# Performance work log

Hardware: AMD Instinct MI355X
Metric: run time of the kernel (lower is better)

Reference implementation:

```python
import jax, jax.numpy as jnp
import numpy as np

B, T, S, H = 4, 2048, 2048, 1024


def setup_inputs() -> dict:
    key = jax.random.key(0)
    k1, k2, k3, k4, k5, k6 = jax.random.split(key, 6)
    scale_w = 1.0 / np.sqrt(H)  # roughly nn.Linear init scale
    return {
        "tar": jax.random.normal(k1, (B, T, H), jnp.float32),
        "src": jax.random.normal(k2, (B, S, H), jnp.float32),
        "ori_src": jax.random.normal(k3, (B, S, H), jnp.float32),
        "Wq": jax.random.normal(k4, (H, H), jnp.float32) * scale_w,
        "Wk": jax.random.normal(k5, (H, H), jnp.float32) * scale_w,
        "Wv": jax.random.normal(k6, (H, H), jnp.float32) * scale_w,
    }


def reference(tar, src, ori_src, Wq, Wk, Wv):
    # nn.Linear(bias=False): y = x @ W.T
    q = src @ Wq.T        # (B, S, H)
    k = tar @ Wk.T        # (B, T, H)
    v = ori_src @ Wv.T    # (B, S, H)
    scaling = jnp.asarray(H ** 0.5, q.dtype)
    # scores[b,t,s] = q[b,s] . k[b,t] / sqrt(H); torch softmax was over dim=-2 (the S axis)
    scores = jnp.einsum('bsh,bth->bts', q, k) / scaling  # (B, T, S)
    attn = jax.nn.softmax(scores, axis=-1)               # softmax over src positions s
    context = jnp.einsum('bts,bsh->bth', attn, v)        # (B, T, H)
    return context, attn
```

## Files before the change

### kernel.cpp

```cpp
#include <hip/hip_runtime.h>

#define BB 4
#define TT 2048
#define SS 2048
#define HH 1024

typedef unsigned short u16;
typedef __attribute__((ext_vector_type(4))) unsigned short u16x4;
typedef __attribute__((ext_vector_type(8))) short bf16x8;
typedef __attribute__((ext_vector_type(4))) float f32x4;

#define TILE_U16 (128 * 32)

__device__ __forceinline__ u16 f2bf(float f) {
    union { float f; unsigned u; } a; a.f = f;
    unsigned r = a.u + 0x7fffu + ((a.u >> 16) & 1u);
    return (u16)(r >> 16);
}
__device__ __forceinline__ float bf2f(u16 h) {
    union { unsigned u; float f; } a; a.u = ((unsigned)h) << 16;
    return a.f;
}


__device__ __forceinline__ void stage_bf16(const u16* gbase, int ld, int row0, int k0,
                                           u16* lds, int tid) {
#pragma unroll
    for (int c = 0; c < 2; ++c) {
        int g = c * 256 + tid;
        int row = g >> 2, col = g & 3;
        const u16* gp = gbase + (size_t)(row0 + row) * ld + k0 + col * 8;
        u16* lp = lds + (size_t)(c * 256 + (tid & ~63)) * 8;
        __builtin_amdgcn_global_load_lds((__attribute__((address_space(1))) const void*)gp,
                                         (__attribute__((address_space(3))) void*)lp,
                                         16, 0, 0);
    }
}

__device__ __forceinline__ void stage_f32(const float* gbase, int ld, int row0, int k0,
                                          u16* lds, int tid) {
#pragma unroll
    for (int c = 0; c < 4; ++c) {
        int f = c * 256 + tid;
        int row = f >> 3, c4 = f & 7;
        const float4 v = *(const float4*)(gbase + (size_t)(row0 + row) * ld + k0 + c4 * 4);
        u16x4 o;
        o.x = f2bf(v.x); o.y = f2bf(v.y); o.z = f2bf(v.z); o.w = f2bf(v.w);
        *(u16x4*)(lds + row * 32 + c4 * 4) = o;
    }
}

__device__ __forceinline__ void mfma_step(const u16* As, const u16* Bs,
                                          f32x4 acc[4][4], int tid) {
    int lane = tid & 63, quad = lane >> 4, l16 = lane & 15;
    int wm = (tid >> 6) & 1, wn = tid >> 7;
    const u16* Ab = As + (wm * 64 + l16) * 32 + quad * 8;
    const u16* Bb = Bs + (wn * 64 + l16) * 32 + quad * 8;
    bf16x8 af[4], bfr[4];
#pragma unroll
    for (int i = 0; i < 4; ++i) af[i] = *(const bf16x8*)(Ab + i * 512);
#pragma unroll
    for (int j = 0; j < 4; ++j) bfr[j] = *(const bf16x8*)(Bb + j * 512);
#pragma unroll
    for (int i = 0; i < 4; ++i)
#pragma unroll
        for (int j = 0; j < 4; ++j)
            acc[i][j] = __builtin_amdgcn_mfma_f32_16x16x32_bf16(af[i], bfr[j], acc[i][j], 0, 0, 0);
}

__device__ __forceinline__ void zero_acc(f32x4 acc[4][4]) {
#pragma unroll
    for (int i = 0; i < 4; ++i)
#pragma unroll
        for (int j = 0; j < 4; ++j)
            acc[i][j] = (f32x4){0.f, 0.f, 0.f, 0.f};
}

__device__ __forceinline__ void gemm_loop_bf16(const u16* A, int lda, int bm,
                                               const u16* B, int ldb, int bn,
                                               int K, u16* As, u16* Bs,
                                               f32x4 acc[4][4], int tid) {
    stage_bf16(A, lda, bm, 0, As, tid);
    stage_bf16(B, ldb, bn, 0, Bs, tid);
    const int kiters = K / 32;
    for (int kit = 0; kit < kiters; ++kit) {
        const int cur = (kit & 1) * TILE_U16, nxt = TILE_U16 - cur;
        __syncthreads();
        if (kit + 1 < kiters) {
            stage_bf16(A, lda, bm, (kit + 1) * 32, As + nxt, tid);
            stage_bf16(B, ldb, bn, (kit + 1) * 32, Bs + nxt, tid);
        }
        mfma_step(As + cur, Bs + cur, acc, tid);
    }
}

__device__ __forceinline__ void gemm_loop_f32a(const float* A, int lda, int bm,
                                               const u16* B, int ldb, int bn,
                                               int K, u16* As, u16* Bs,
                                               f32x4 acc[4][4], int tid) {
    stage_f32(A, lda, bm, 0, As, tid);
    stage_bf16(B, ldb, bn, 0, Bs, tid);
    const int kiters = K / 32;
    for (int kit = 0; kit < kiters; ++kit) {
        const int cur = (kit & 1) * TILE_U16, nxt = TILE_U16 - cur;
        __syncthreads();
        if (kit + 1 < kiters) {
            stage_f32(A, lda, bm, (kit + 1) * 32, As + nxt, tid);
            stage_bf16(B, ldb, bn, (kit + 1) * 32, Bs + nxt, tid);
        }
        mfma_step(As + cur, Bs + cur, acc, tid);
    }
}


__global__ __launch_bounds__(256) void cvt3_kernel(const float* __restrict__ p0,
                                                   const float* __restrict__ p1,
                                                   const float* __restrict__ p2,
                                                   u16* __restrict__ o0,
                                                   u16* __restrict__ o1,
                                                   u16* __restrict__ o2) {
    const int z = blockIdx.y;
    const float* in = (z == 0) ? p0 : (z == 1) ? p1 : p2;
    u16* out = (z == 0) ? o0 : (z == 1) ? o1 : o2;
    int i = (blockIdx.x * 256 + threadIdx.x) * 4;
    float4 v = *(const float4*)(in + i);
    u16x4 o;
    o.x = f2bf(v.x); o.y = f2bf(v.y); o.z = f2bf(v.z); o.w = f2bf(v.w);
    *(u16x4*)(out + i) = o;
}

__global__ __launch_bounds__(256) void cvt_kernel(const float* __restrict__ in,
                                                  u16* __restrict__ out) {
    int i = (blockIdx.x * 256 + threadIdx.x) * 4;
    float4 v = *(const float4*)(in + i);
    u16x4 o;
    o.x = f2bf(v.x); o.y = f2bf(v.y); o.z = f2bf(v.z); o.w = f2bf(v.w);
    *(u16x4*)(out + i) = o;
}

__global__ __launch_bounds__(256) void zero_kernel(float* __restrict__ p) {
    int i = (blockIdx.x * 256 + threadIdx.x) * 4;
    *(float4*)(p + i) = (float4){0.f, 0.f, 0.f, 0.f};
}


__device__ __forceinline__ void stage_half(const u16* g, int ld, u16* lds, int tid) {
#pragma unroll
    for (int c = 0; c < 2; ++c) {
        int gr = c * 512 + tid;
        int r = gr >> 3, k8 = gr & 7;
        const u16* gp = g + (size_t)r * ld + ((k8 ^ (r & 7)) << 3);
        u16* lp = lds + (size_t)(c * 512 + (tid & ~63)) * 8;
        __builtin_amdgcn_global_load_lds((__attribute__((address_space(1))) const void*)gp,
                                         (__attribute__((address_space(3))) void*)lp,
                                         16, 0, 0);
    }
}

#define G_RD_A(dst, Abp, qm)                                                  \
    _Pragma("unroll") for (int i = 0; i < 4; ++i) {                           \
        const u16* _p = (Abp) + ((qm) * 64 + i * 16 + l16) * 64;              \
        dst[i][0] = *(const bf16x8*)(_p + co0);                               \
        dst[i][1] = *(const bf16x8*)(_p + co1);                               \
    }

#define G_RD_B(dst, Bbp, qn)                                                  \
    _Pragma("unroll") for (int j = 0; j < J2; ++j) {                          \
        const u16* _p = (Bbp) + (rB0 + (qn) * J2 * 16 + j * 16 + l16) * 64;   \
        dst[j][0] = *(const bf16x8*)(_p + co0);                               \
        dst[j][1] = *(const bf16x8*)(_p + co1);                               \
    }

#define G_MM(af, bf, qm, qn)                                                  \
    __builtin_amdgcn_s_setprio(1);                                            \
    _Pragma("unroll") for (int i = 0; i < 4; ++i)                             \
        _Pragma("unroll") for (int j = 0; j < J2; ++j) {                      \
            acc[(qm) * 4 + i][(qn) * J2 + j] =                                \
                __builtin_amdgcn_mfma_f32_16x16x32_bf16(                      \
                    af[i][0], bf[j][0], acc[(qm) * 4 + i][(qn) * J2 + j], 0, 0, 0); \
            acc[(qm) * 4 + i][(qn) * J2 + j] =                                \
                __builtin_amdgcn_mfma_f32_16x16x32_bf16(                      \
                    af[i][1], bf[j][1], acc[(qm) * 4 + i][(qn) * J2 + j], 0, 0, 0); \
        }                                                                     \
    __builtin_amdgcn_s_setprio(0);

template <int BN>
__device__ __forceinline__ void g256_loop(const u16* __restrict__ A, int lda,
                                          const u16* __restrict__ B, int ldb, int K,
                                          u16* sm, f32x4 (&acc)[8][BN / 64], int tid) {
    constexpr int J2 = BN / 128;
    constexpr int ATILE = 16384;
    constexpr int BTILE = BN * 64;
    u16* As = sm;
    u16* Bs = sm + 2 * ATILE;
    const int lane = tid & 63, wid = tid >> 6;
    const int wm = wid >> 2, wn = wid & 3;
    const int l16 = lane & 15, quad = lane >> 4;
    const int co0 = (quad ^ (l16 & 7)) * 8;
    const int co1 = ((4 | quad) ^ (l16 & 7)) * 8;
    const int rB0 = (BN == 256) ? (wn & 1) * 64 : wn * 32;
    const int NT = K >> 6;

#pragma unroll
    for (int i = 0; i < 8; ++i)
#pragma unroll
        for (int j = 0; j < BN / 64; ++j) acc[i][j] = (f32x4){0.f, 0.f, 0.f, 0.f};

    stage_half(A, lda, As, tid);
    stage_half(A + (size_t)128 * lda, lda, As + 8192, tid);
    stage_half(B, ldb, Bs, tid);
    if (BN == 256) stage_half(B + (size_t)128 * ldb, ldb, Bs + 8192, tid);
    stage_half(A + 64, lda, As + ATILE, tid);
    stage_half(A + (size_t)128 * lda + 64, lda, As + ATILE + 8192, tid);
    asm volatile("s_waitcnt vmcnt(4)" ::: "memory");
    __builtin_amdgcn_s_barrier();
    __builtin_amdgcn_sched_barrier(0);

    const u16* Aw = As + wm * 8192;
    const u16* Bw = Bs + ((BN == 256) ? (wn >> 1) * 8192 : 0);

    bf16x8 a0[4][2], a1[4][2], b0[J2][2], b1[J2][2];
    {
        const u16* Ab = Aw;
        const u16* Bb = Bw;
        G_RD_A(a0, Ab, 0)
        G_RD_B(b0, Bb, 0)
    }

    for (int t = 0; t < NT; ++t) {
        const u16* Ab = Aw + (t & 1) * ATILE;
        const u16* Bb = Bw + (t & 1) * BTILE;
        const int nx = (t + 1) & 1;
        G_RD_A(a1, Ab, 1)
        if (t + 1 < NT) stage_half(B + (size_t)(t + 1) * 64, ldb, Bs + nx * BTILE, tid);
        __builtin_amdgcn_sched_barrier(0);
        G_MM(a0, b0, 0, 0)
        G_RD_B(b1, Bb, 1)
        if (BN == 256 && t + 1 < NT)
            stage_half(B + (size_t)128 * ldb + (size_t)(t + 1) * 64, ldb,
                       Bs + nx * BTILE + 8192, tid);
        __builtin_amdgcn_sched_barrier(0);
        G_MM(a1, b0, 1, 0)
        asm volatile("s_waitcnt lgkmcnt(0)" ::: "memory");
        __builtin_amdgcn_sched_barrier(0);
        __builtin_amdgcn_s_barrier();
        if (t + 2 < NT) {
            stage_half(A + (size_t)(t + 2) * 64, lda, As + (t & 1) * ATILE, tid);
            stage_half(A + (size_t)128 * lda + (size_t)(t + 2) * 64, lda,
                       As + (t & 1) * ATILE + 8192, tid);
        }
        __builtin_amdgcn_sched_barrier(0);
        G_MM(a0, b1, 0, 1)
        if (t + 2 < NT) asm volatile("s_waitcnt vmcnt(4)" ::: "memory");
        else            asm volatile("s_waitcnt vmcnt(0)" ::: "memory");
        __builtin_amdgcn_s_barrier();
        __builtin_amdgcn_sched_barrier(0);
        if (t + 1 < NT) {
            const u16* An = Aw + nx * ATILE;
            const u16* Bn = Bw + nx * BTILE;
            G_RD_A(a0, An, 0)
            G_RD_B(b0, Bn, 0)
        }
        __builtin_amdgcn_sched_barrier(0);
        G_MM(a1, b1, 1, 1)
    }
}

__global__ __launch_bounds__(512, 2) void proj256_kernel(
        const u16* __restrict__ A0, const u16* __restrict__ A1, const u16* __restrict__ A2,
        const u16* __restrict__ W0, const u16* __restrict__ W1, const u16* __restrict__ W2,
        u16* __restrict__ qb, u16* __restrict__ kb, u16* __restrict__ vT) {
    __shared__ u16 sm[2 * 16384 + 2 * 128 * 64];
    const int bid = blockIdx.x;
    const int wg = (bid & 7) * 96 + (bid >> 3);
    const int z = wg >> 8, rr = wg & 255;
    const int by = rr >> 3, bx = rr & 7;
    const u16* A = ((z == 0) ? A0 : (z == 1) ? A1 : A2) + (size_t)(by * 256) * HH;
    const u16* W = ((z == 0) ? W0 : (z == 1) ? W1 : W2) + (size_t)(bx * 128) * HH;
    const int tid = threadIdx.x;
    f32x4 acc[8][2];
    g256_loop<128>(A, HH, W, HH, HH, sm, acc, tid);

    const int lane = tid & 63, quad = lane >> 4, l16 = lane & 15, wid = tid >> 6;
    const int wm = wid >> 2, wn = wid & 3;
    const int m0 = by * 256 + wm * 128, n0 = bx * 128 + wn * 32;
    if (z < 2) {
        u16* C = z ? kb : qb;
#pragma unroll
        for (int i = 0; i < 8; ++i)
#pragma unroll
            for (int j = 0; j < 2; ++j) {
                const int m = m0 + i * 16 + quad * 4;
                const int n = n0 + j * 16 + l16;
#pragma unroll
                for (int r = 0; r < 4; ++r)
                    C[(size_t)(m + r) * HH + n] = f2bf(acc[i][j][r]);
            }
    } else {
#pragma unroll
        for (int i = 0; i < 8; ++i)
#pragma unroll
            for (int j = 0; j < 2; ++j) {
                const int m = m0 + i * 16 + quad * 4;
                const int n = n0 + j * 16 + l16;
                u16x4 o;
                o.x = f2bf(acc[i][j][0]); o.y = f2bf(acc[i][j][1]);
                o.z = f2bf(acc[i][j][2]); o.w = f2bf(acc[i][j][3]);
                *(u16x4*)(vT + (size_t)n * (BB * SS) + m) = o;
            }
    }
}

__global__ __launch_bounds__(512, 2) void scores256_kernel(
        const u16* __restrict__ qb, const u16* __restrict__ kb,
        u16* __restrict__ eb, float* __restrict__ rowsum) {
    __shared__ u16 sm[2 * 16384 + 2 * 256 * 64];
    const int bid = blockIdx.x;
    const int wg = (bid & 7) * 32 + (bid >> 3);
    const int b = wg >> 6, by = (wg >> 3) & 7, bx = wg & 7;
    const u16* A = kb + (size_t)b * TT * HH + (size_t)(by * 256) * HH;
    const u16* Q = qb + (size_t)b * SS * HH + (size_t)(bx * 256) * HH;
    const int tid = threadIdx.x;
    f32x4 acc[8][4];
    g256_loop<256>(A, HH, Q, HH, HH, sm, acc, tid);

    const int lane = tid & 63, quad = lane >> 4, l16 = lane & 15, wid = tid >> 6;
    const int wm = wid >> 2, wn = wid & 3;
    const int m0 = by * 256 + wm * 128, n0 = bx * 256 + wn * 64;
#pragma unroll
    for (int i = 0; i < 8; ++i)
#pragma unroll
        for (int j = 0; j < 4; ++j)
#pragma unroll
            for (int r = 0; r < 4; ++r)
                acc[i][j][r] = __expf(acc[i][j][r] * 0.03125f);
    u16* E = eb + (size_t)b * TT * SS;
#pragma unroll
    for (int i = 0; i < 8; ++i)
#pragma unroll
        for (int j = 0; j < 4; ++j) {
            const int m = m0 + i * 16 + quad * 4;
            const int n = n0 + j * 16 + l16;
#pragma unroll
            for (int r = 0; r < 4; ++r)
                E[(size_t)(m + r) * SS + n] = f2bf(acc[i][j][r]);
        }
    const size_t Rb = (size_t)b * TT + m0 + quad * 4;
#pragma unroll
    for (int i = 0; i < 8; ++i)
#pragma unroll
        for (int r = 0; r < 4; ++r) {
            float s = acc[i][0][r] + acc[i][1][r] + acc[i][2][r] + acc[i][3][r];
            s += __shfl_xor(s, 1, 64);
            s += __shfl_xor(s, 2, 64);
            s += __shfl_xor(s, 4, 64);
            s += __shfl_xor(s, 8, 64);
            if (l16 == 0) atomicAdd(&rowsum[Rb + i * 16 + r], s);
        }
}

__global__ __launch_bounds__(512, 2) void ctx256_kernel(
        const u16* __restrict__ eb, const u16* __restrict__ vT,
        const float* __restrict__ rowsum, float* __restrict__ out) {
    __shared__ u16 sm[2 * 16384 + 2 * 128 * 64];
    const int bid = blockIdx.x;
    const int wg = (bid & 7) * 32 + (bid >> 3);
    const int b = wg >> 6, by = (wg >> 3) & 7, bx = wg & 7;
    const u16* A = eb + (size_t)b * TT * SS + (size_t)(by * 256) * SS;
    const u16* V = vT + (size_t)b * SS + (size_t)(bx * 128) * (size_t)(BB * SS);
    const int tid = threadIdx.x;
    f32x4 acc[8][2];
    g256_loop<128>(A, SS, V, BB * SS, SS, sm, acc, tid);

    const int lane = tid & 63, quad = lane >> 4, l16 = lane & 15, wid = tid >> 6;
    const int wm = wid >> 2, wn = wid & 3;
    const int m0 = by * 256 + wm * 128, n0 = bx * 128 + wn * 32;
    float* C = out + (size_t)b * TT * HH;
    const float* RS = rowsum + (size_t)b * TT;
#pragma unroll
    for (int i = 0; i < 8; ++i)
#pragma unroll
        for (int r = 0; r < 4; ++r) {
            const int m = m0 + i * 16 + quad * 4 + r;
            const float scl = 1.0f / RS[m];
#pragma unroll
            for (int j = 0; j < 2; ++j)
                C[(size_t)m * HH + n0 + j * 16 + l16] = acc[i][j][r] * scl;
        }
}


template <int AF32, int NZ>
__global__ __launch_bounds__(256, 4) void proj_kernel(const float* __restrict__ F0,
                                                      const float* __restrict__ F1,
                                                      const float* __restrict__ F2,
                                                      const u16* __restrict__ A0,
                                                      const u16* __restrict__ A1,
                                                      const u16* __restrict__ A2,
                                                      const u16* __restrict__ W0,
                                                      const u16* __restrict__ W1,
                                                      const u16* __restrict__ W2,
                                                      u16* __restrict__ qb,
                                                      u16* __restrict__ kb,
                                                      u16* __restrict__ vT,
                                                      int zbase) {
    __shared__ u16 As[2 * TILE_U16];
    __shared__ u16 Bs[2 * TILE_U16];
    const int bid = blockIdx.x;
    const int xcd = bid & 7, slot = bid >> 3;
    const int bx = slot & 7;
    const int grp = xcd * (NZ * 8) + (slot >> 3);
    const int z = zbase + (NZ == 3 ? (grp >> 6) : 0);
    const int by = grp & 63;

    const float* AF = (z == 0) ? F0 : (z == 1) ? F1 : F2;
    const u16* AB = (z == 0) ? A0 : (z == 1) ? A1 : A2;
    const u16* W = (z == 0) ? W0 : (z == 1) ? W1 : W2;
    const int bm = by * 128, bn = bx * 128;
    const int tid = threadIdx.x;

    f32x4 acc[4][4];
    zero_acc(acc);
    if (AF32) gemm_loop_f32a(AF, HH, bm, W, HH, bn, HH, As, Bs, acc, tid);
    else      gemm_loop_bf16(AB, HH, bm, W, HH, bn, HH, As, Bs, acc, tid);

    const int lane = tid & 63, quad = lane >> 4, l16 = lane & 15;
    const int wm = (tid >> 6) & 1, wn = tid >> 7;
    const int m0 = bm + wm * 64, n0 = bn + wn * 64;
    if (z < 2) {
        u16* C = (z == 0) ? qb : kb;
#pragma unroll
        for (int i = 0; i < 4; ++i)
#pragma unroll
            for (int j = 0; j < 4; ++j) {
                int m = m0 + i * 16 + quad * 4;
                int n = n0 + j * 16 + l16;
#pragma unroll
                for (int r = 0; r < 4; ++r)
                    C[(size_t)(m + r) * HH + n] = f2bf(acc[i][j][r]);
            }
    } else {
#pragma unroll
        for (int i = 0; i < 4; ++i)
#pragma unroll
            for (int j = 0; j < 4; ++j) {
                int m = m0 + i * 16 + quad * 4;
                int n = n0 + j * 16 + l16;
                u16x4 o;
                o.x = f2bf(acc[i][j][0]); o.y = f2bf(acc[i][j][1]);
                o.z = f2bf(acc[i][j][2]); o.w = f2bf(acc[i][j][3]);
                *(u16x4*)(vT + (size_t)n * (BB * SS) + m) = o;
            }
    }
}

template <int FUSE>
__global__ __launch_bounds__(256, 4) void scores_kernel(const u16* __restrict__ qb,
                                                        const u16* __restrict__ kb,
                                                        float* __restrict__ attn,
                                                        u16* __restrict__ eb,
                                                        float* __restrict__ rowsum) {
    __shared__ u16 As[2 * TILE_U16];
    __shared__ u16 Bs[2 * TILE_U16];
    const int bid = blockIdx.x;
    const int xcd = bid & 7, slot = bid >> 3;
    const int bx = slot & 15;
    const int grp = xcd * 8 + (slot >> 4);
    const int b = grp >> 4, by = grp & 15;

    const u16* A = kb + (size_t)b * TT * HH;
    const u16* Bq = qb + (size_t)b * SS * HH;
    const int bm = by * 128, bn = bx * 128;
    const int tid = threadIdx.x;

    f32x4 acc[4][4];
    zero_acc(acc);
    gemm_loop_bf16(A, HH, bm, Bq, HH, bn, HH, As, Bs, acc, tid);

    const int lane = tid & 63, quad = lane >> 4, l16 = lane & 15;
    const int wm = (tid >> 6) & 1, wn = tid >> 7;
    const int m0 = bm + wm * 64, n0 = bn + wn * 64;

    if (FUSE) {
#pragma unroll
        for (int i = 0; i < 4; ++i)
#pragma unroll
            for (int j = 0; j < 4; ++j)
#pragma unroll
                for (int r = 0; r < 4; ++r)
                    acc[i][j][r] = __expf(acc[i][j][r] * 0.03125f);
        u16* E = eb + (size_t)b * TT * SS;
#pragma unroll
        for (int i = 0; i < 4; ++i)
#pragma unroll
            for (int j = 0; j < 4; ++j) {
                int m = m0 + i * 16 + quad * 4;
                int n = n0 + j * 16 + l16;
#pragma unroll
                for (int r = 0; r < 4; ++r)
                    E[(size_t)(m + r) * SS + n] = f2bf(acc[i][j][r]);
            }
        const size_t Rb = (size_t)b * TT + m0 + quad * 4;
#pragma unroll
        for (int i = 0; i < 4; ++i)
#pragma unroll
            for (int r = 0; r < 4; ++r) {
                float s = acc[i][0][r] + acc[i][1][r] + acc[i][2][r] + acc[i][3][r];
                s += __shfl_xor(s, 1, 64);
                s += __shfl_xor(s, 2, 64);
                s += __shfl_xor(s, 4, 64);
                s += __shfl_xor(s, 8, 64);
                if (l16 == 0) atomicAdd(&rowsum[Rb + i * 16 + r], s);
            }
    } else {
        float* C = attn + (size_t)b * TT * SS;
#pragma unroll
        for (int i = 0; i < 4; ++i)
#pragma unroll
            for (int j = 0; j < 4; ++j) {
                int m = m0 + i * 16 + quad * 4;
                int n = n0 + j * 16 + l16;
#pragma unroll
                for (int r = 0; r < 4; ++r)
                    C[(size_t)(m + r) * SS + n] = acc[i][j][r] * 0.03125f;
            }
    }
}

__global__ __launch_bounds__(256) void norm_kernel(const u16* __restrict__ eb,
                                                   const float* __restrict__ rowsum,
                                                   float* __restrict__ attn) {
    const size_t row = blockIdx.x;
    const float inv = 1.0f / rowsum[row];
    const u16* p = eb + row * SS;
    float* o = attn + row * SS;
    const int tid = threadIdx.x;
#pragma unroll
    for (int c = 0; c < 2; ++c) {
        u16x4 v = *(const u16x4*)(p + c * 1024 + tid * 4);
        float4 f;
        f.x = bf2f(v.x) * inv; f.y = bf2f(v.y) * inv;
        f.z = bf2f(v.z) * inv; f.w = bf2f(v.w) * inv;
        *(float4*)(o + c * 1024 + tid * 4) = f;
    }
}

__global__ __launch_bounds__(256) void softmax_kernel(float* __restrict__ attn,
                                                      u16* __restrict__ attn_bf) {
    const size_t row = blockIdx.x;
    float* p = attn + row * SS;
    const int tid = threadIdx.x;
    float4 a = *(float4*)(p + tid * 4);
    float4 b = *(float4*)(p + 1024 + tid * 4);

    float m = fmaxf(fmaxf(fmaxf(a.x, a.y), fmaxf(a.z, a.w)),
                    fmaxf(fmaxf(b.x, b.y), fmaxf(b.z, b.w)));
#pragma unroll
    for (int off = 32; off > 0; off >>= 1) m = fmaxf(m, __shfl_xor(m, off, 64));
    __shared__ float rmax[4], rsum[4];
    if ((tid & 63) == 0) rmax[tid >> 6] = m;
    __syncthreads();
    m = fmaxf(fmaxf(rmax[0], rmax[1]), fmaxf(rmax[2], rmax[3]));

    a.x = __expf(a.x - m); a.y = __expf(a.y - m);
    a.z = __expf(a.z - m); a.w = __expf(a.w - m);
    b.x = __expf(b.x - m); b.y = __expf(b.y - m);
    b.z = __expf(b.z - m); b.w = __expf(b.w - m);
    float s = a.x + a.y + a.z + a.w + b.x + b.y + b.z + b.w;
#pragma unroll
    for (int off = 32; off > 0; off >>= 1) s += __shfl_xor(s, off, 64);
    if ((tid & 63) == 0) rsum[tid >> 6] = s;
    __syncthreads();
    s = rsum[0] + rsum[1] + rsum[2] + rsum[3];
    float inv = 1.0f / s;

    a.x *= inv; a.y *= inv; a.z *= inv; a.w *= inv;
    b.x *= inv; b.y *= inv; b.z *= inv; b.w *= inv;
    *(float4*)(p + tid * 4) = a;
    *(float4*)(p + 1024 + tid * 4) = b;

    if (attn_bf) {
        u16* pb = attn_bf + row * SS;
        u16x4 oa, ob;
        oa.x = f2bf(a.x); oa.y = f2bf(a.y); oa.z = f2bf(a.z); oa.w = f2bf(a.w);
        ob.x = f2bf(b.x); ob.y = f2bf(b.y); ob.z = f2bf(b.z); ob.w = f2bf(b.w);
        *(u16x4*)(pb + tid * 4) = oa;
        *(u16x4*)(pb + 1024 + tid * 4) = ob;
    }
}

template <int AF32, int SCALE>
__global__ __launch_bounds__(256, 4) void ctx_kernel(const float* __restrict__ attnF,
                                                     const u16* __restrict__ attnB,
                                                     const u16* __restrict__ vT,
                                                     const float* __restrict__ rowsum,
                                                     float* __restrict__ out) {
    __shared__ u16 As[2 * TILE_U16];
    __shared__ u16 Bs[2 * TILE_U16];
    const int bid = blockIdx.x;
    const int xcd = bid & 7, slot = bid >> 3;
    const int bx = slot & 7;
    const int grp = xcd * 8 + (slot >> 3);
    const int b = grp >> 4, by = grp & 15;

    const float* AF = attnF + (size_t)b * TT * SS;
    const u16* AB = attnB + (size_t)b * TT * SS;
    const u16* Bv = vT + (size_t)b * SS;
    float* C = out + (size_t)b * TT * HH;
    const int bm = by * 128, bn = bx * 128;
    const int tid = threadIdx.x;

    f32x4 acc[4][4];
    zero_acc(acc);
    if (AF32) gemm_loop_f32a(AF, SS, bm, Bv, BB * SS, bn, SS, As, Bs, acc, tid);
    else      gemm_loop_bf16(AB, SS, bm, Bv, BB * SS, bn, SS, As, Bs, acc, tid);

    const int lane = tid & 63, quad = lane >> 4, l16 = lane & 15;
    const int wm = (tid >> 6) & 1, wn = tid >> 7;
    const int m0 = bm + wm * 64, n0 = bn + wn * 64;
#pragma unroll
    for (int i = 0; i < 4; ++i)
#pragma unroll
        for (int r = 0; r < 4; ++r) {
            int m = m0 + i * 16 + quad * 4 + r;
            float scl = 1.0f;
            if (SCALE) scl = 1.0f / rowsum[(size_t)b * TT + m];
#pragma unroll
            for (int j = 0; j < 4; ++j) {
                int n = n0 + j * 16 + l16;
                C[(size_t)m * HH + n] = acc[i][j][r] * scl;
            }
        }
}

extern "C" void kernel_launch(void* const* d_in, const int* in_sizes, int n_in,
                              void* d_out, int out_size, void* d_ws, size_t ws_size,
                              hipStream_t stream) {
    const float* tar = (const float*)d_in[0];
    const float* src = (const float*)d_in[1];
    const float* ori = (const float*)d_in[2];
    const float* Wq  = (const float*)d_in[3];
    const float* Wk  = (const float*)d_in[4];
    const float* Wv  = (const float*)d_in[5];

    float* ctx_out  = (float*)d_out;
    float* attn_out = ctx_out + (size_t)BB * TT * HH;

    const size_t M1 = 1024 * 1024;
    u16* ws  = (u16*)d_ws;
    u16* qb  = ws;
    u16* kb  = ws + 8 * M1;
    u16* vT  = ws + 16 * M1;
    u16* wqb = ws + 24 * M1;
    u16* wkb = ws + 25 * M1;
    u16* wvb = ws + 26 * M1;
    u16* inb = ws + 27 * M1;
    u16* eb = inb;
    float* rowsum = (float*)wqb;
    u16* attn_bf = qb;

    const size_t need_fused = (27 + 24) * M1 * 2;
    const size_t need_split = (27 + 8) * M1 * 2;
    const int mode = (ws_size >= need_fused) ? 0 : (ws_size >= need_split) ? 1 : 2;

    cvt3_kernel<<<dim3(1024, 3), 256, 0, stream>>>(Wq, Wk, Wv, wqb, wkb, wvb);

    if (mode == 0) {
        u16* srcb = inb;
        u16* tarb = inb + 8 * M1;
        u16* orib = inb + 16 * M1;
        cvt3_kernel<<<dim3(8192, 3), 256, 0, stream>>>(src, tar, ori, srcb, tarb, orib);
        proj256_kernel<<<768, 512, 0, stream>>>(srcb, tarb, orib, wqb, wkb, wvb, qb, kb, vT);
        zero_kernel<<<8, 256, 0, stream>>>(rowsum);
        scores256_kernel<<<256, 512, 0, stream>>>(qb, kb, eb, rowsum);
        norm_kernel<<<BB * TT, 256, 0, stream>>>(eb, rowsum, attn_out);
        ctx256_kernel<<<256, 512, 0, stream>>>(eb, vT, rowsum, ctx_out);
    } else if (mode == 1) {
        const float* fin[3] = {src, tar, ori};
        for (int z = 0; z < 3; ++z) {
            cvt_kernel<<<8192, 256, 0, stream>>>(fin[z], inb);
            proj_kernel<0, 1><<<512, 256, 0, stream>>>(
                nullptr, nullptr, nullptr, inb, inb, inb, wqb, wkb, wvb, qb, kb, vT, z);
        }
        scores_kernel<0><<<1024, 256, 0, stream>>>(qb, kb, attn_out, nullptr, nullptr);
        softmax_kernel<<<BB * TT, 256, 0, stream>>>(attn_out, attn_bf);
        ctx_kernel<0, 0><<<512, 256, 0, stream>>>(nullptr, attn_bf, vT, nullptr, ctx_out);
    } else {
        proj_kernel<1, 3><<<1536, 256, 0, stream>>>(
            src, tar, ori, nullptr, nullptr, nullptr, wqb, wkb, wvb, qb, kb, vT, 0);
        scores_kernel<0><<<1024, 256, 0, stream>>>(qb, kb, attn_out, nullptr, nullptr);
        softmax_kernel<<<BB * TT, 256, 0, stream>>>(attn_out, nullptr);
        ctx_kernel<1, 0><<<512, 256, 0, stream>>>(attn_out, nullptr, vT, nullptr, ctx_out);
    }
}
```

Before: 345.1 us.

## Restructure GEMM main loop schedule and use 256x256 tiles in projection

Rewrites the shared GEMM inner loop so each MFMA quadrant is preceded by a barrier-plus-lgkmcnt wait, with LDS fragment reads and global staging interleaved differently across the four sub-steps and no cross-iteration register prefetch. Separately, the projection kernel switches from 256x128 to 256x256 tiles, halving the grid to 384 blocks and doubling the LDS footprint and accumulators. The goal is better MFMA/LDS overlap and more data reuse in the projection. The cost is more barriers per iteration, more registers per thread, and lower block count and occupancy, since the loop change also affects the scores and context kernels that share it.

```diff
diff --git a/kernel.cpp b/kernel.cpp
--- a/kernel.cpp
+++ b/kernel.cpp
@@ -183,6 +183,12 @@
                     af[i][1], bf[j][1], acc[(qm) * 4 + i][(qn) * J2 + j], 0, 0, 0); \
         }                                                                     \
     __builtin_amdgcn_s_setprio(0);
+
+#define G_SYNC_PRE_MM()                                                       \
+    __builtin_amdgcn_sched_barrier(0);                                        \
+    __builtin_amdgcn_s_barrier();                                             \
+    asm volatile("s_waitcnt lgkmcnt(0)" ::: "memory");                        \
+    __builtin_amdgcn_sched_barrier(0);
 
 template <int BN>
 __device__ __forceinline__ void g256_loop(const u16* __restrict__ A, int lda,
@@ -216,53 +222,44 @@
     __builtin_amdgcn_s_barrier();
     __builtin_amdgcn_sched_barrier(0);
 
-    const u16* Aw = As + wm * 8192;
-    const u16* Bw = Bs + ((BN == 256) ? (wn >> 1) * 8192 : 0);
+    const u16* AwBase = As + wm * 8192;
+    const u16* BwBase = Bs + ((BN == 256) ? (wn >> 1) * 8192 : 0);
 
     bf16x8 a0[4][2], a1[4][2], b0[J2][2], b1[J2][2];
-    {
-        const u16* Ab = Aw;
-        const u16* Bb = Bw;
+
+    for (int t = 0; t < NT; ++t) {
+        const u16* Ab = AwBase + (t & 1) * ATILE;
+        const u16* Bb = BwBase + (t & 1) * BTILE;
+        const int curA = (t & 1) * ATILE;
+        const int nxB = ((t + 1) & 1) * BTILE;
         G_RD_A(a0, Ab, 0)
         G_RD_B(b0, Bb, 0)
-    }
-
-    for (int t = 0; t < NT; ++t) {
-        const u16* Ab = Aw + (t & 1) * ATILE;
-        const u16* Bb = Bw + (t & 1) * BTILE;
-        const int nx = (t + 1) & 1;
+        if (t + 1 < NT) stage_half(B + (size_t)(t + 1) * 64, ldb, Bs + nxB, tid);
+        G_SYNC_PRE_MM()
+        G_MM(a0, b0, 0, 0)
+        __builtin_amdgcn_s_barrier();
         G_RD_A(a1, Ab, 1)
-        if (t + 1 < NT) stage_half(B + (size_t)(t + 1) * 64, ldb, Bs + nx * BTILE, tid);
-        __builtin_amdgcn_sched_barrier(0);
-        G_MM(a0, b0, 0, 0)
-        G_RD_B(b1, Bb, 1)
         if (BN == 256 && t + 1 < NT)
             stage_half(B + (size_t)128 * ldb + (size_t)(t + 1) * 64, ldb,
-                       Bs + nx * BTILE + 8192, tid);
-        __builtin_amdgcn_sched_barrier(0);
+                       Bs + nxB + 8192, tid);
+        G_SYNC_PRE_MM()
         G_MM(a1, b0, 1, 0)
-        asm volatile("s_waitcnt lgkmcnt(0)" ::: "memory");
-        __builtin_amdgcn_sched_barrier(0);
         __builtin_amdgcn_s_barrier();
-        if (t + 2 < NT) {
-            stage_half(A + (size_t)(t + 2) * 64, lda, As + (t & 1) * ATILE, tid);
+        G_RD_B(b1, Bb, 1)
+        if (t + 2 < NT)
+            stage_half(A + (size_t)(t + 2) * 64, lda, As + curA, tid);
+        G_SYNC_PRE_MM()
+        G_MM(a1, b1, 1, 1)
+        __builtin_amdgcn_s_barrier();
+        if (t + 2 < NT)
             stage_half(A + (size_t)128 * lda + (size_t)(t + 2) * 64, lda,
-                       As + (t & 1) * ATILE + 8192, tid);
-        }
+                       As + curA + 8192, tid);
         __builtin_amdgcn_sched_barrier(0);
         G_MM(a0, b1, 0, 1)
-        if (t + 2 < NT) asm volatile("s_waitcnt vmcnt(4)" ::: "memory");
-        else            asm volatile("s_waitcnt vmcnt(0)" ::: "memory");
+        if (t + 2 < NT)      asm volatile("s_waitcnt vmcnt(4)" ::: "memory");
+        else if (t + 1 < NT) asm volatile("s_waitcnt vmcnt(0)" ::: "memory");
         __builtin_amdgcn_s_barrier();
         __builtin_amdgcn_sched_barrier(0);
-        if (t + 1 < NT) {
-            const u16* An = Aw + nx * ATILE;
-            const u16* Bn = Bw + nx * BTILE;
-            G_RD_A(a0, An, 0)
-            G_RD_B(b0, Bn, 0)
-        }
-        __builtin_amdgcn_sched_barrier(0);
-        G_MM(a1, b1, 1, 1)
     }
 }
 
@@ -270,26 +267,26 @@
         const u16* __restrict__ A0, const u16* __restrict__ A1, const u16* __restrict__ A2,
         const u16* __restrict__ W0, const u16* __restrict__ W1, const u16* __restrict__ W2,
         u16* __restrict__ qb, u16* __restrict__ kb, u16* __restrict__ vT) {
-    __shared__ u16 sm[2 * 16384 + 2 * 128 * 64];
+    __shared__ u16 sm[2 * 16384 + 2 * 256 * 64];
     const int bid = blockIdx.x;
-    const int wg = (bid & 7) * 96 + (bid >> 3);
-    const int z = wg >> 8, rr = wg & 255;
-    const int by = rr >> 3, bx = rr & 7;
+    const int wg = (bid & 7) * 48 + (bid >> 3);
+    const int z = wg >> 7, rr = wg & 127;
+    const int by = rr >> 2, bx = rr & 3;
     const u16* A = ((z == 0) ? A0 : (z == 1) ? A1 : A2) + (size_t)(by * 256) * HH;
-    const u16* W = ((z == 0) ? W0 : (z == 1) ? W1 : W2) + (size_t)(bx * 128) * HH;
-    const int tid = threadIdx.x;
-    f32x4 acc[8][2];
-    g256_loop<128>(A, HH, W, HH, HH, sm, acc, tid);
+    const u16* W = ((z == 0) ? W0 : (z == 1) ? W1 : W2) + (size_t)(bx * 256) * HH;
+    const int tid = threadIdx.x;
+    f32x4 acc[8][4];
+    g256_loop<256>(A, HH, W, HH, HH, sm, acc, tid);
 
     const int lane = tid & 63, quad = lane >> 4, l16 = lane & 15, wid = tid >> 6;
     const int wm = wid >> 2, wn = wid & 3;
-    const int m0 = by * 256 + wm * 128, n0 = bx * 128 + wn * 32;
+    const int m0 = by * 256 + wm * 128, n0 = bx * 256 + wn * 64;
     if (z < 2) {
         u16* C = z ? kb : qb;
 #pragma unroll
         for (int i = 0; i < 8; ++i)
 #pragma unroll
-            for (int j = 0; j < 2; ++j) {
+            for (int j = 0; j < 4; ++j) {
                 const int m = m0 + i * 16 + quad * 4;
                 const int n = n0 + j * 16 + l16;
 #pragma unroll
@@ -300,7 +297,7 @@
 #pragma unroll
         for (int i = 0; i < 8; ++i)
 #pragma unroll
-            for (int j = 0; j < 2; ++j) {
+            for (int j = 0; j < 4; ++j) {
                 const int m = m0 + i * 16 + quad * 4;
                 const int n = n0 + j * 16 + l16;
                 u16x4 o;
@@ -670,7 +667,7 @@
         u16* tarb = inb + 8 * M1;
         u16* orib = inb + 16 * M1;
         cvt3_kernel<<<dim3(8192, 3), 256, 0, stream>>>(src, tar, ori, srcb, tarb, orib);
-        proj256_kernel<<<768, 512, 0, stream>>>(srcb, tarb, orib, wqb, wkb, wvb, qb, kb, vT);
+        proj256_kernel<<<384, 512, 0, stream>>>(srcb, tarb, orib, wqb, wkb, wvb, qb, kb, vT);
         zero_kernel<<<8, 256, 0, stream>>>(rowsum);
         scores256_kernel<<<256, 512, 0, stream>>>(qb, kb, eb, rowsum);
         norm_kernel<<<BB * TT, 256, 0, stream>>>(eb, rowsum, attn_out);
```

After: 342.1 us. Within noise of the previous version (-0.9%).
